# Kernel tuning notes

Hardware: AMD Instinct MI355X
Metric: run time of the kernel (lower is better)

## Reference

```python
import jax, jax.numpy as jnp
import numpy as np
import math

N, E, IN, C, H, ED, B = 50000, 800000, 64, 32, 4, 1, 64
HC = H * C
EPS = 1e-5


def setup_inputs() -> dict:
    key = jax.random.key(0)
    ks = jax.random.split(key, 16)
    def lin(k, fan_in, fan_out):
        s = 1.0 / math.sqrt(fan_in)
        return jax.random.normal(k, (fan_in, fan_out), jnp.float32) * s
    inp = {
        "x": jax.random.normal(ks[0], (N, IN), jnp.float32),
        "edge_index": jax.random.randint(ks[1], (2, E), 0, N, jnp.int64),
        "edge_attr": jax.random.normal(ks[2], (E, ED), jnp.float32),
        "batch_index": jnp.sort(jax.random.randint(ks[3], (N,), 0, B, jnp.int64)),
        # TransformerConv params
        "Wq": lin(ks[4], IN, HC), "bq": jnp.zeros((HC,), jnp.float32),
        "Wk": lin(ks[5], IN, HC), "bk": jnp.zeros((HC,), jnp.float32),
        "Wv": lin(ks[6], IN, HC), "bv": jnp.zeros((HC,), jnp.float32),
        "We": lin(ks[7], ED, HC), "be": jnp.zeros((HC,), jnp.float32),
        "Wskip": lin(ks[8], IN, HC), "bskip": jnp.zeros((HC,), jnp.float32),
        "Wbeta": lin(ks[9], 3 * HC, 1),
        # post linear: H*C -> C
        "Wlin": lin(ks[10], HC, C), "blin": jnp.zeros((C,), jnp.float32),
        # GraphNorm params
        "gn_weight": jnp.ones((C,), jnp.float32),
        "gn_bias": jnp.zeros((C,), jnp.float32),
        "gn_mean_scale": jnp.ones((C,), jnp.float32),
    }
    return inp


def reference(x, edge_index, edge_attr, batch_index, Wq, bq, Wk, bk, Wv, bv,
              We, be, Wskip, bskip, Wbeta, Wlin, blin,
              gn_weight, gn_bias, gn_mean_scale):
    src, dst = edge_index[0], edge_index[1]
    # dense projections [N, H, C]
    q = (x @ Wq + bq).reshape(N, H, C)
    k = (x @ Wk + bk).reshape(N, H, C)
    v = (x @ Wv + bv).reshape(N, H, C)
    e = (edge_attr @ We + be).reshape(E, H, C)
    # per-edge attention logits [E, H]
    k_e = k[src] + e
    alpha = jnp.einsum('ehc,ehc->eh', q[dst], k_e) / math.sqrt(C)
    # segment softmax over incoming edges of each dst node
    m = jax.ops.segment_max(alpha, dst, num_segments=N)  # [N, H]
    a = jnp.exp(alpha - m[dst])
    denom = jax.ops.segment_sum(a, dst, num_segments=N)  # [N, H]
    a = a / jnp.maximum(denom, 1e-16)[dst]
    # (dropout p=0.3 on attention is a no-op in eval mode)
    msg = (v[src] + e) * a[:, :, None]                    # [E, H, C]
    out = jax.ops.segment_sum(msg, dst, num_segments=N).reshape(N, HC)
    # beta-gated skip connection
    x_r = x @ Wskip + bskip                               # [N, HC]
    beta = jax.nn.sigmoid(jnp.concatenate([out, x_r, out - x_r], -1) @ Wbeta)
    out = beta * x_r + (1.0 - beta) * out
    # linear + relu
    h = jax.nn.relu(out @ Wlin + blin)                    # [N, C]
    # GraphNorm over per-graph segments
    ones = jnp.ones((N, 1), h.dtype)
    cnt = jax.ops.segment_sum(ones, batch_index, num_segments=B)  # [B, 1]
    cnt = jnp.maximum(cnt, 1.0)
    mean = jax.ops.segment_sum(h, batch_index, num_segments=B) / cnt
    centered = h - mean[batch_index] * gn_mean_scale
    var = jax.ops.segment_sum(centered * centered, batch_index, num_segments=B) / cnt
    std = jnp.sqrt(var + EPS)
    return gn_weight * centered / std[batch_index] + gn_bias
```

## Files before the change

### kernel.cpp

```cpp
#include <hip/hip_runtime.h>
#include <math.h>

static constexpr int kN  = 50000;
static constexpr int kE  = 800000;
static constexpr int kC  = 32;
static constexpr int kH  = 4;
static constexpr int kHC = 128;
static constexpr int kB  = 64;
static constexpr int kNB = (kN + 255) / 256;
static constexpr int kMB64 = (kN + 63) / 64;

typedef __attribute__((ext_vector_type(8))) short bf16x8;
typedef __attribute__((ext_vector_type(4))) float f32x4;

__device__ __forceinline__ unsigned short f2bf(float f) {
    unsigned u = __float_as_uint(f);
    unsigned r = (u + 0x7FFFu + ((u >> 16) & 1u)) >> 16;
    return (unsigned short)r;
}
__device__ __forceinline__ float blo(unsigned u) { return __uint_as_float(u << 16); }
__device__ __forceinline__ float bhi(unsigned u) { return __uint_as_float(u & 0xFFFF0000u); }

__global__ __launch_bounds__(256) void hist_packw_kernel(
    const int* __restrict__ ei, int* __restrict__ deg,
    const float* __restrict__ Wq, const float* __restrict__ Wk,
    const float* __restrict__ Wv, const float* __restrict__ Wskip,
    uint4* __restrict__ wtf)
{
    if (blockIdx.x < 16) {
        int tid = blockIdx.x * 256 + threadIdx.x;
        int f = tid >> 6, l = tid & 63;
        int m = f >> 4, c = (f >> 1) & 7, kk = f & 1;
        int col = c * 16 + (l & 15);
        int k0  = kk * 32 + (l >> 4) * 8;
        const float* Wm = (m == 0) ? Wq : (m == 1) ? Wk : (m == 2) ? Wv : Wskip;
        unsigned p[4];
#pragma unroll
        for (int j = 0; j < 4; ++j) {
            unsigned lo = f2bf(Wm[(k0 + 2 * j) * kHC + col]);
            unsigned hi = f2bf(Wm[(k0 + 2 * j + 1) * kHC + col]);
            p[j] = lo | (hi << 16);
        }
        wtf[f * 64 + l] = make_uint4(p[0], p[1], p[2], p[3]);
        return;
    }
    int i = (blockIdx.x - 16) * 256 + threadIdx.x;
    if (i < kE) atomicAdd(&deg[ei[kE + i]], 1);
}

__global__ __launch_bounds__(256) void proj_scanA_kernel(
    const float4* __restrict__ x4,
    const float* __restrict__ bq, const float* __restrict__ bk,
    const float* __restrict__ bv, const float* __restrict__ bskip,
    const uint4* __restrict__ wtf,
    unsigned short* __restrict__ qxb, unsigned short* __restrict__ kvb,
    const int* __restrict__ deg, int* __restrict__ bsum)
{
    __shared__ int sh4[4];
    if (blockIdx.x >= kMB64) {
        int bid = blockIdx.x - kMB64;
        int i = bid * 256 + threadIdx.x;
        int v = (i < kN) ? deg[i] : 0;
#pragma unroll
        for (int s = 1; s < 64; s <<= 1) v += __shfl_xor(v, s);
        if ((threadIdx.x & 63) == 0) sh4[threadIdx.x >> 6] = v;
        __syncthreads();
        if (threadIdx.x == 0) bsum[bid] = sh4[0] + sh4[1] + sh4[2] + sh4[3];
        return;
    }
    const int t = threadIdx.x;
    const int w = t >> 6;
    const int l = t & 63;
    const int l15 = l & 15, l16 = l >> 4;
    const int n0 = blockIdx.x * 64;

    bf16x8 bf[8][2];
#pragma unroll
    for (int c = 0; c < 8; ++c)
#pragma unroll
        for (int kk = 0; kk < 2; ++kk)
            bf[c][kk] = __builtin_bit_cast(bf16x8, wtf[(unsigned)((w * 16 + c * 2 + kk) * 64 + l)]);

    const float* Bm = (w == 0) ? bq : (w == 1) ? bk : (w == 2) ? bv : bskip;
    float bias[8];
#pragma unroll
    for (int c = 0; c < 8; ++c) bias[c] = Bm[c * 16 + l15];

    unsigned short* dst = (w == 0 || w == 3) ? qxb : kvb;
    const int add4 = (w >= 2) ? 4 : 0;

    for (int rt = 0; rt < 2; ++rt) {
        const int r0 = n0 + rt * 32 + l15;
        const int r1 = r0 + 16;
        f32x4 acc[2][8];
#pragma unroll
        for (int r = 0; r < 2; ++r)
#pragma unroll
            for (int c = 0; c < 8; ++c)
                acc[r][c] = (f32x4){bias[c], bias[c], bias[c], bias[c]};
#pragma unroll
        for (int kk = 0; kk < 2; ++kk) {
            float4 xa0 = make_float4(0.f,0.f,0.f,0.f), xb0 = xa0, xa1 = xa0, xb1 = xa0;
            if (r0 < kN) {
                xa0 = x4[(size_t)r0 * 16 + kk * 8 + l16 * 2];
                xb0 = x4[(size_t)r0 * 16 + kk * 8 + l16 * 2 + 1];
            }
            if (r1 < kN) {
                xa1 = x4[(size_t)r1 * 16 + kk * 8 + l16 * 2];
                xb1 = x4[(size_t)r1 * 16 + kk * 8 + l16 * 2 + 1];
            }
            uint4 u0 = make_uint4(
                f2bf(xa0.x) | ((unsigned)f2bf(xa0.y) << 16),
                f2bf(xa0.z) | ((unsigned)f2bf(xa0.w) << 16),
                f2bf(xb0.x) | ((unsigned)f2bf(xb0.y) << 16),
                f2bf(xb0.z) | ((unsigned)f2bf(xb0.w) << 16));
            uint4 u1 = make_uint4(
                f2bf(xa1.x) | ((unsigned)f2bf(xa1.y) << 16),
                f2bf(xa1.z) | ((unsigned)f2bf(xa1.w) << 16),
                f2bf(xb1.x) | ((unsigned)f2bf(xb1.y) << 16),
                f2bf(xb1.z) | ((unsigned)f2bf(xb1.w) << 16));
            bf16x8 a0 = __builtin_bit_cast(bf16x8, u0);
            bf16x8 a1 = __builtin_bit_cast(bf16x8, u1);
#pragma unroll
            for (int c = 0; c < 8; ++c) {
                acc[0][c] = __builtin_amdgcn_mfma_f32_16x16x32_bf16(a0, bf[c][kk], acc[0][c], 0, 0, 0);
                acc[1][c] = __builtin_amdgcn_mfma_f32_16x16x32_bf16(a1, bf[c][kk], acc[1][c], 0, 0, 0);
            }
        }
#pragma unroll
        for (int r = 0; r < 2; ++r) {
#pragma unroll
            for (int j = 0; j < 4; ++j) {
                int node = n0 + rt * 32 + r * 16 + l16 * 4 + j;
                bool valid = (node < kN) && ((l & 1) == 0);
                size_t base = (size_t)node * 128;
#pragma unroll
                for (int c = 0; c < 8; ++c) {
                    float v0 = acc[r][c][j];
                    float v1 = __shfl_xor(v0, 1);
                    if (valid) {
                        int jcol = c * 16 + l15;
                        int gpos = ((jcol >> 2) << 3) | (jcol & 3);
                        unsigned pk = f2bf(v0) | ((unsigned)f2bf(v1) << 16);
                        ((unsigned*)dst)[base + ((gpos + add4) >> 1)] = pk;
                    }
                }
            }
        }
    }
}

__global__ __launch_bounds__(256) void scanC2_kernel(
    const int* __restrict__ deg, const int* __restrict__ bsum,
    int* __restrict__ rowptr, int* __restrict__ cursor)
{
    __shared__ int bsh[256];
    __shared__ int sh[256];
    const int t = threadIdx.x, i = blockIdx.x * 256 + t;
    int bv = (t < kNB) ? bsum[t] : 0;
    bsh[t] = bv; __syncthreads();
    for (int off = 1; off < 256; off <<= 1) {
        int u = (t >= off) ? bsh[t - off] : 0;
        __syncthreads();
        bsh[t] += u;
        __syncthreads();
    }
    const int bofs = (blockIdx.x == 0) ? 0 : bsh[blockIdx.x - 1];
    if (blockIdx.x == 0 && t == 0) rowptr[kN] = bsh[kNB - 1];
    int v = (i < kN) ? deg[i] : 0;
    sh[t] = v; __syncthreads();
    for (int off = 1; off < 256; off <<= 1) {
        int u = (t >= off) ? sh[t - off] : 0;
        __syncthreads();
        sh[t] += u;
        __syncthreads();
    }
    if (i < kN) {
        int ex = sh[t] - v + bofs;
        rowptr[i] = ex;
        cursor[i] = ex;
    }
}

__global__ __launch_bounds__(256) void scatter_kernel(
    const int* __restrict__ ei, const float* __restrict__ ea,
    int* __restrict__ cursor, unsigned* __restrict__ csr)
{
    int i = blockIdx.x * 256 + threadIdx.x;
    if (i >= kE) return;
    int dst = ei[kE + i];
    int slot = atomicAdd(&cursor[dst], 1);
    csr[slot] = (unsigned)ei[i] | ((unsigned)f2bf(ea[i]) << 16);
}

__global__ __launch_bounds__(512) void node_attn_kernel(
    const int* __restrict__ rowptr, const unsigned* __restrict__ csr,
    const unsigned short* __restrict__ qxb, const unsigned short* __restrict__ kvb,
    const float* __restrict__ We, const float* __restrict__ be,
    const float* __restrict__ Wbeta, const float* __restrict__ Wlin,
    const float* __restrict__ blin, float* __restrict__ hbuf)
{
    __shared__ float wlS[kHC * kC];
    __shared__ float wbS[3 * kHC];
    __shared__ float oshS[8][kHC];
    const int t = threadIdx.x, wv = t >> 6, lane = t & 63;
    for (int i = t; i < kHC * kC; i += 512) wlS[i] = Wlin[i];
    for (int i = t; i < 3 * kHC; i += 512) wbS[i] = Wbeta[i];
    __syncthreads();

    const int node = blockIdx.x * 8 + wv;
    const int half = lane >> 5;
    const int sl   = lane & 31;
    const int ch   = sl * 4;
    const float4 we4 = *(const float4*)&We[ch];
    const float4 be4 = *(const float4*)&be[ch];
    const float4 wbA = *(const float4*)&wbS[ch];
    const float4 wbB = *(const float4*)&wbS[kHC + ch];
    const float4 wbC = *(const float4*)&wbS[2 * kHC + ch];
    const float blc = blin[sl];
    const float A2 = 0.17677669529663687f * 1.44269504088896341f;

    const uint4 qx = *((const uint4*)(qxb + (size_t)node * 256) + sl);
    const float q0 = blo(qx.x), q1 = bhi(qx.x), q2v = blo(qx.y), q3 = bhi(qx.y);
    const float xr0 = blo(qx.z), xr1 = bhi(qx.z), xr2 = blo(qx.w), xr3 = bhi(qx.w);
    float qw = q0 * we4.x + q1 * we4.y + q2v * we4.z + q3 * we4.w;
    float qe = q0 * be4.x + q1 * be4.y + q2v * be4.z + q3 * be4.w;
    qw += __shfl_xor(qw, 1); qe += __shfl_xor(qe, 1);
    qw += __shfl_xor(qw, 2); qe += __shfl_xor(qe, 2);
    qw += __shfl_xor(qw, 4); qe += __shfl_xor(qe, 4);
    const float qwA = qw * A2, qbA = qe * A2;

    float ss = 0.f, swa = 0.f;
    float ax0 = 0.f, ax1 = 0.f, ax2 = 0.f, ax3 = 0.f;
    const int beg = rowptr[node], end = rowptr[node + 1];
    int e = beg;
    for (; e + 3 < end; e += 4) {
        unsigned cA = csr[e + half];
        unsigned cB = csr[e + 2 + half];
        float aA = bhi(cA), aB = bhi(cB);
        const uint4 uA = *((const uint4*)(kvb + (size_t)(cA & 0xFFFFu) * 256) + sl);
        const uint4 uB = *((const uint4*)(kvb + (size_t)(cB & 0xFFFFu) * 256) + sl);
        float pA = fmaf(q3, bhi(uA.y), fmaf(q2v, blo(uA.y), fmaf(q1, bhi(uA.x), q0 * blo(uA.x))));
        float pB = fmaf(q3, bhi(uB.y), fmaf(q2v, blo(uB.y), fmaf(q1, bhi(uB.x), q0 * blo(uB.x))));
        pA += __shfl_xor(pA, 1); pB += __shfl_xor(pB, 1);
        pA += __shfl_xor(pA, 2); pB += __shfl_xor(pB, 2);
        pA += __shfl_xor(pA, 4); pB += __shfl_xor(pB, 4);
        float eA = __builtin_amdgcn_exp2f(fmaf(pA, A2, fmaf(aA, qwA, qbA)));
        float eB = __builtin_amdgcn_exp2f(fmaf(pB, A2, fmaf(aB, qwA, qbA)));
        ss  += eA + eB;
        swa = fmaf(eA, aA, fmaf(eB, aB, swa));
        ax0 = fmaf(eA, blo(uA.z), fmaf(eB, blo(uB.z), ax0));
        ax1 = fmaf(eA, bhi(uA.z), fmaf(eB, bhi(uB.z), ax1));
        ax2 = fmaf(eA, blo(uA.w), fmaf(eB, blo(uB.w), ax2));
        ax3 = fmaf(eA, bhi(uA.w), fmaf(eB, bhi(uB.w), ax3));
    }
    for (; e < end; e += 2) {
        int idx = e + half;
        bool valid = idx < end;
        unsigned cA = csr[valid ? idx : end - 1];
        float aA = bhi(cA);
        const uint4 uA = *((const uint4*)(kvb + (size_t)(cA & 0xFFFFu) * 256) + sl);
        float pA = fmaf(q3, bhi(uA.y), fmaf(q2v, blo(uA.y), fmaf(q1, bhi(uA.x), q0 * blo(uA.x))));
        pA += __shfl_xor(pA, 1);
        pA += __shfl_xor(pA, 2);
        pA += __shfl_xor(pA, 4);
        float eA = valid ? __builtin_amdgcn_exp2f(fmaf(pA, A2, fmaf(aA, qwA, qbA))) : 0.f;
        ss  += eA;
        swa = fmaf(eA, aA, swa);
        ax0 = fmaf(eA, blo(uA.z), ax0);
        ax1 = fmaf(eA, bhi(uA.z), ax1);
        ax2 = fmaf(eA, blo(uA.w), ax2);
        ax3 = fmaf(eA, bhi(uA.w), ax3);
    }
    ss  += __shfl_xor(ss , 32);
    swa += __shfl_xor(swa, 32);
    ax0 += __shfl_xor(ax0, 32);
    ax1 += __shfl_xor(ax1, 32);
    ax2 += __shfl_xor(ax2, 32);
    ax3 += __shfl_xor(ax3, 32);

    float rcp = 1.f / fmaxf(ss, 1e-16f);
    float v0 = fmaf(swa, we4.x, fmaf(ss, be4.x, ax0)) * rcp;
    float v1 = fmaf(swa, we4.y, fmaf(ss, be4.y, ax1)) * rcp;
    float v2 = fmaf(swa, we4.z, fmaf(ss, be4.z, ax2)) * rcp;
    float v3 = fmaf(swa, we4.w, fmaf(ss, be4.w, ax3)) * rcp;
    float part = wbA.x * v0 + wbA.y * v1 + wbA.z * v2 + wbA.w * v3
               + wbB.x * xr0 + wbB.y * xr1 + wbB.z * xr2 + wbB.w * xr3
               + wbC.x * (v0 - xr0) + wbC.y * (v1 - xr1)
               + wbC.z * (v2 - xr2) + wbC.w * (v3 - xr3);
    part += __shfl_xor(part, 1);
    part += __shfl_xor(part, 2);
    part += __shfl_xor(part, 4);
    part += __shfl_xor(part, 8);
    part += __shfl_xor(part, 16);
    float beta = 1.f / (1.f + __expf(-part));
    float o0 = beta * xr0 + (1.f - beta) * v0;
    float o1 = beta * xr1 + (1.f - beta) * v1;
    float o2 = beta * xr2 + (1.f - beta) * v2;
    float o3 = beta * xr3 + (1.f - beta) * v3;
    if (half == 0) *(float4*)&oshS[wv][ch] = make_float4(o0, o1, o2, o3);
    __builtin_amdgcn_wave_barrier();
    float hp = 0.f;
#pragma unroll
    for (int jj = 0; jj < 64; ++jj) {
        int j = half * 64 + jj;
        hp = fmaf(oshS[wv][j], wlS[j * kC + sl], hp);
    }
    hp += __shfl_xor(hp, 32);
    if (lane < 32) hbuf[(size_t)node * kC + sl] = fmaxf(hp + blc, 0.f);
}

__global__ __launch_bounds__(512) void gn_kernel(
    const float* __restrict__ hbuf, const int* __restrict__ batch,
    const float* __restrict__ gms,
    const float* __restrict__ gw, const float* __restrict__ gb,
    float* __restrict__ out)
{
    const int g = blockIdx.x;
    const int t = threadIdx.x;
    __shared__ int se[2];
    __shared__ float s1[16][kC], s2[16][kC];
    __shared__ float msS[kC], rsS[kC];
    if (t < 2) {
        int target = g + t;
        int lo = 0, hi = kN;
        while (lo < hi) { int mid = (lo + hi) >> 1; if (batch[mid] < target) lo = mid + 1; else hi = mid; }
        se[t] = lo;
    }
    __syncthreads();
    int start = se[0], end = se[1];
    float cnt = fmaxf((float)(end - start), 1.f);
    int c = t & 31, r = t >> 5;
    float a = 0.f, b = 0.f;
    for (int n = start + r; n < end; n += 16) {
        float v = hbuf[(size_t)n * kC + c];
        a += v; b = fmaf(v, v, b);
    }
    s1[r][c] = a; s2[r][c] = b;
    __syncthreads();
    if (t < kC) {
        float sa = 0.f, sb = 0.f;
#pragma unroll
        for (int i = 0; i < 16; ++i) { sa += s1[i][t]; sb += s2[i][t]; }
        float mean = sa / cnt;
        float ms   = mean * gms[t];
        float var  = sb / cnt - 2.f * ms * mean + ms * ms;
        msS[t] = ms;
        rsS[t] = rsqrtf(var + 1e-5f);
    }
    __syncthreads();
    float ms = msS[c], rs = rsS[c], w = gw[c], bb = gb[c];
    for (int n = start + r; n < end; n += 16) {
        float v = hbuf[(size_t)n * kC + c];
        out[(size_t)n * kC + c] = fmaf(w * (v - ms), rs, bb);
    }
}

extern "C" void kernel_launch(void* const* d_in, const int* in_sizes, int n_in,
                              void* d_out, int out_size, void* d_ws, size_t ws_size,
                              hipStream_t stream) {
    (void)in_sizes; (void)n_in; (void)out_size; (void)ws_size;
    const float* x     = (const float*)d_in[0];
    const int*   ei    = (const int*)d_in[1];
    const float* ea    = (const float*)d_in[2];
    const int*   batch = (const int*)d_in[3];
    const float* Wq    = (const float*)d_in[4];
    const float* bq    = (const float*)d_in[5];
    const float* Wk    = (const float*)d_in[6];
    const float* bk    = (const float*)d_in[7];
    const float* Wv    = (const float*)d_in[8];
    const float* bv    = (const float*)d_in[9];
    const float* We    = (const float*)d_in[10];
    const float* be    = (const float*)d_in[11];
    const float* Wskip = (const float*)d_in[12];
    const float* bskip = (const float*)d_in[13];
    const float* Wbeta = (const float*)d_in[14];
    const float* Wlin  = (const float*)d_in[15];
    const float* blin  = (const float*)d_in[16];
    const float* gw    = (const float*)d_in[17];
    const float* gb    = (const float*)d_in[18];
    const float* gms   = (const float*)d_in[19];
    float* out = (float*)d_out;

    char* ws = (char*)d_ws;
    unsigned* csr = (unsigned*)ws;        ws += (size_t)kE * 4;
    unsigned short* qxb = (unsigned short*)ws; ws += (size_t)kN * 256 * 2;
    unsigned short* kvb = (unsigned short*)ws; ws += (size_t)kN * 256 * 2;
    float* hbuf   = (float*)ws;           ws += (size_t)kN * kC * 4;
    int*   deg    = (int*)ws;             ws += (size_t)kN * 4;
    int*   cursor = (int*)ws;             ws += (size_t)kN * 4;
    int*   rowptr = (int*)ws;             ws += (size_t)(kN + 1) * 4;
    int*   bsum   = (int*)ws;             ws += (size_t)kNB * 4;
    uint4* wtf    = (uint4*)ws;           ws += (size_t)64 * 64 * 16;

    hipMemsetAsync(deg, 0, (size_t)kN * 4, stream);

    hist_packw_kernel<<<16 + (kE + 255) / 256, 256, 0, stream>>>(
        ei, deg, Wq, Wk, Wv, Wskip, wtf);
    proj_scanA_kernel<<<kMB64 + kNB, 256, 0, stream>>>(
        (const float4*)x, bq, bk, bv, bskip, wtf, qxb, kvb, deg, bsum);
    scanC2_kernel<<<kNB, 256, 0, stream>>>(deg, bsum, rowptr, cursor);
    scatter_kernel<<<(kE + 255) / 256, 256, 0, stream>>>(ei, ea, cursor, csr);
    node_attn_kernel<<<kN / 8, 512, 0, stream>>>(
        rowptr, csr, qxb, kvb, We, be, Wbeta, Wlin, blin, hbuf);
    gn_kernel<<<kB, 512, 0, stream>>>(hbuf, batch, gms, gw, gb, out);
}
```

Baseline: 222.2 us.

## Store keys as FP8 in a 384-byte KV row and fuse projection with scatter

```diff
diff --git a/kernel.cpp b/kernel.cpp
--- a/kernel.cpp
+++ b/kernel.cpp
@@ -9,9 +9,12 @@
 static constexpr int kB  = 64;
 static constexpr int kNB = (kN + 255) / 256;
 static constexpr int kMB64 = (kN + 63) / 64;
+static constexpr int kSB  = (kE + 255) / 256;
+static constexpr int kKVROW = 384;
 
 typedef __attribute__((ext_vector_type(8))) short bf16x8;
 typedef __attribute__((ext_vector_type(4))) float f32x4;
+typedef __attribute__((ext_vector_type(2))) float f32x2;
 
 __device__ __forceinline__ unsigned short f2bf(float f) {
     unsigned u = __float_as_uint(f);
@@ -48,24 +51,67 @@
     if (i < kE) atomicAdd(&deg[ei[kE + i]], 1);
 }
 
-__global__ __launch_bounds__(256) void proj_scanA_kernel(
+__global__ __launch_bounds__(256) void scanA_kernel(
+    const int* __restrict__ deg, int* __restrict__ bsum)
+{
+    __shared__ int sh4[4];
+    int i = blockIdx.x * 256 + threadIdx.x;
+    int v = (i < kN) ? deg[i] : 0;
+#pragma unroll
+    for (int s = 1; s < 64; s <<= 1) v += __shfl_xor(v, s);
+    if ((threadIdx.x & 63) == 0) sh4[threadIdx.x >> 6] = v;
+    __syncthreads();
+    if (threadIdx.x == 0) bsum[blockIdx.x] = sh4[0] + sh4[1] + sh4[2] + sh4[3];
+}
+
+__global__ __launch_bounds__(256) void scanC2_kernel(
+    const int* __restrict__ deg, const int* __restrict__ bsum,
+    int* __restrict__ rowptr, int* __restrict__ cursor)
+{
+    __shared__ int bsh[256];
+    __shared__ int sh[256];
+    const int t = threadIdx.x, i = blockIdx.x * 256 + t;
+    int bv = (t < kNB) ? bsum[t] : 0;
+    bsh[t] = bv; __syncthreads();
+    for (int off = 1; off < 256; off <<= 1) {
+        int u = (t >= off) ? bsh[t - off] : 0;
+        __syncthreads();
+        bsh[t] += u;
+        __syncthreads();
+    }
+    const int bofs = (blockIdx.x == 0) ? 0 : bsh[blockIdx.x - 1];
+    if (blockIdx.x == 0 && t == 0) rowptr[kN] = bsh[kNB - 1];
+    int v = (i < kN) ? deg[i] : 0;
+    sh[t] = v; __syncthreads();
+    for (int off = 1; off < 256; off <<= 1) {
+        int u = (t >= off) ? sh[t - off] : 0;
+        __syncthreads();
+        sh[t] += u;
+        __syncthreads();
+    }
+    if (i < kN) {
+        int ex = sh[t] - v + bofs;
+        rowptr[i] = ex;
+        cursor[i] = ex;
+    }
+}
+
+__global__ __launch_bounds__(256) void proj_scatter_kernel(
     const float4* __restrict__ x4,
     const float* __restrict__ bq, const float* __restrict__ bk,
     const float* __restrict__ bv, const float* __restrict__ bskip,
     const uint4* __restrict__ wtf,
-    unsigned short* __restrict__ qxb, unsigned short* __restrict__ kvb,
-    const int* __restrict__ deg, int* __restrict__ bsum)
-{
-    __shared__ int sh4[4];
+    unsigned short* __restrict__ qxb, unsigned char* __restrict__ kvb,
+    const int* __restrict__ ei, const float* __restrict__ ea,
+    int* __restrict__ cursor, unsigned* __restrict__ csr)
+{
     if (blockIdx.x >= kMB64) {
-        int bid = blockIdx.x - kMB64;
-        int i = bid * 256 + threadIdx.x;
-        int v = (i < kN) ? deg[i] : 0;
-#pragma unroll
-        for (int s = 1; s < 64; s <<= 1) v += __shfl_xor(v, s);
-        if ((threadIdx.x & 63) == 0) sh4[threadIdx.x >> 6] = v;
-        __syncthreads();
-        if (threadIdx.x == 0) bsum[bid] = sh4[0] + sh4[1] + sh4[2] + sh4[3];
+        int i = (blockIdx.x - kMB64) * 256 + threadIdx.x;
+        if (i < kE) {
+            int dst = ei[kE + i];
+            int slot = atomicAdd(&cursor[dst], 1);
+            csr[slot] = (unsigned)ei[i] | ((unsigned)f2bf(ea[i]) << 16);
+        }
         return;
     }
     const int t = threadIdx.x;
@@ -86,7 +132,6 @@
 #pragma unroll
     for (int c = 0; c < 8; ++c) bias[c] = Bm[c * 16 + l15];
 
-    unsigned short* dst = (w == 0 || w == 3) ? qxb : kvb;
     const int add4 = (w >= 2) ? 4 : 0;
 
     for (int rt = 0; rt < 2; ++rt) {
@@ -133,16 +178,24 @@
             for (int j = 0; j < 4; ++j) {
                 int node = n0 + rt * 32 + r * 16 + l16 * 4 + j;
                 bool valid = (node < kN) && ((l & 1) == 0);
-                size_t base = (size_t)node * 128;
 #pragma unroll
                 for (int c = 0; c < 8; ++c) {
                     float v0 = acc[r][c][j];
                     float v1 = __shfl_xor(v0, 1);
                     if (valid) {
                         int jcol = c * 16 + l15;
-                        int gpos = ((jcol >> 2) << 3) | (jcol & 3);
-                        unsigned pk = f2bf(v0) | ((unsigned)f2bf(v1) << 16);
-                        ((unsigned*)dst)[base + ((gpos + add4) >> 1)] = pk;
+                        if (w == 0 || w == 3) {
+                            int gpos = ((jcol >> 2) << 3) | (jcol & 3);
+                            unsigned pk = f2bf(v0) | ((unsigned)f2bf(v1) << 16);
+                            ((unsigned*)qxb)[(size_t)node * 128 + ((gpos + add4) >> 1)] = pk;
+                        } else if (w == 1) {
+                            unsigned short us = (unsigned short)
+                                __builtin_amdgcn_cvt_pk_fp8_f32(v0, v1, 0, false);
+                            *(unsigned short*)(kvb + (size_t)node * kKVROW + jcol) = us;
+                        } else {
+                            unsigned pk = f2bf(v0) | ((unsigned)f2bf(v1) << 16);
+                            *(unsigned*)(kvb + (size_t)node * kKVROW + 128 + 2 * jcol) = pk;
+                        }
                     }
                 }
             }
@@ -150,52 +203,9 @@
     }
 }
 
-__global__ __launch_bounds__(256) void scanC2_kernel(
-    const int* __restrict__ deg, const int* __restrict__ bsum,
-    int* __restrict__ rowptr, int* __restrict__ cursor)
-{
-    __shared__ int bsh[256];
-    __shared__ int sh[256];
-    const int t = threadIdx.x, i = blockIdx.x * 256 + t;
-    int bv = (t < kNB) ? bsum[t] : 0;
-    bsh[t] = bv; __syncthreads();
-    for (int off = 1; off < 256; off <<= 1) {
-        int u = (t >= off) ? bsh[t - off] : 0;
-        __syncthreads();
-        bsh[t] += u;
-        __syncthreads();
-    }
-    const int bofs = (blockIdx.x == 0) ? 0 : bsh[blockIdx.x - 1];
-    if (blockIdx.x == 0 && t == 0) rowptr[kN] = bsh[kNB - 1];
-    int v = (i < kN) ? deg[i] : 0;
-    sh[t] = v; __syncthreads();
-    for (int off = 1; off < 256; off <<= 1) {
-        int u = (t >= off) ? sh[t - off] : 0;
-        __syncthreads();
-        sh[t] += u;
-        __syncthreads();
-    }
-    if (i < kN) {
-        int ex = sh[t] - v + bofs;
-        rowptr[i] = ex;
-        cursor[i] = ex;
-    }
-}
-
-__global__ __launch_bounds__(256) void scatter_kernel(
-    const int* __restrict__ ei, const float* __restrict__ ea,
-    int* __restrict__ cursor, unsigned* __restrict__ csr)
-{
-    int i = blockIdx.x * 256 + threadIdx.x;
-    if (i >= kE) return;
-    int dst = ei[kE + i];
-    int slot = atomicAdd(&cursor[dst], 1);
-    csr[slot] = (unsigned)ei[i] | ((unsigned)f2bf(ea[i]) << 16);
-}
-
 __global__ __launch_bounds__(512) void node_attn_kernel(
     const int* __restrict__ rowptr, const unsigned* __restrict__ csr,
-    const unsigned short* __restrict__ qxb, const unsigned short* __restrict__ kvb,
+    const unsigned short* __restrict__ qxb, const unsigned char* __restrict__ kvb,
     const float* __restrict__ We, const float* __restrict__ be,
     const float* __restrict__ Wbeta, const float* __restrict__ Wlin,
     const float* __restrict__ blin, float* __restrict__ hbuf)
@@ -238,10 +248,18 @@
         unsigned cA = csr[e + half];
         unsigned cB = csr[e + 2 + half];
         float aA = bhi(cA), aB = bhi(cB);
-        const uint4 uA = *((const uint4*)(kvb + (size_t)(cA & 0xFFFFu) * 256) + sl);
-        const uint4 uB = *((const uint4*)(kvb + (size_t)(cB & 0xFFFFu) * 256) + sl);
-        float pA = fmaf(q3, bhi(uA.y), fmaf(q2v, blo(uA.y), fmaf(q1, bhi(uA.x), q0 * blo(uA.x))));
-        float pB = fmaf(q3, bhi(uB.y), fmaf(q2v, blo(uB.y), fmaf(q1, bhi(uB.x), q0 * blo(uB.x))));
+        const unsigned char* rA = kvb + (size_t)(cA & 0xFFFFu) * kKVROW;
+        const unsigned char* rB = kvb + (size_t)(cB & 0xFFFFu) * kKVROW;
+        unsigned kuA = *(const unsigned*)(rA + sl * 4);
+        unsigned kuB = *(const unsigned*)(rB + sl * 4);
+        uint2 vuA = *(const uint2*)(rA + 128 + sl * 8);
+        uint2 vuB = *(const uint2*)(rB + 128 + sl * 8);
+        f32x2 kA0 = __builtin_amdgcn_cvt_pk_f32_fp8(kuA, false);
+        f32x2 kA1 = __builtin_amdgcn_cvt_pk_f32_fp8(kuA, true);
+        f32x2 kB0 = __builtin_amdgcn_cvt_pk_f32_fp8(kuB, false);
+        f32x2 kB1 = __builtin_amdgcn_cvt_pk_f32_fp8(kuB, true);
+        float pA = fmaf(q3, kA1.y, fmaf(q2v, kA1.x, fmaf(q1, kA0.y, q0 * kA0.x)));
+        float pB = fmaf(q3, kB1.y, fmaf(q2v, kB1.x, fmaf(q1, kB0.y, q0 * kB0.x)));
         pA += __shfl_xor(pA, 1); pB += __shfl_xor(pB, 1);
         pA += __shfl_xor(pA, 2); pB += __shfl_xor(pB, 2);
         pA += __shfl_xor(pA, 4); pB += __shfl_xor(pB, 4);
@@ -249,28 +267,32 @@
         float eB = __builtin_amdgcn_exp2f(fmaf(pB, A2, fmaf(aB, qwA, qbA)));
         ss  += eA + eB;
         swa = fmaf(eA, aA, fmaf(eB, aB, swa));
-        ax0 = fmaf(eA, blo(uA.z), fmaf(eB, blo(uB.z), ax0));
-        ax1 = fmaf(eA, bhi(uA.z), fmaf(eB, bhi(uB.z), ax1));
-        ax2 = fmaf(eA, blo(uA.w), fmaf(eB, blo(uB.w), ax2));
-        ax3 = fmaf(eA, bhi(uA.w), fmaf(eB, bhi(uB.w), ax3));
+        ax0 = fmaf(eA, blo(vuA.x), fmaf(eB, blo(vuB.x), ax0));
+        ax1 = fmaf(eA, bhi(vuA.x), fmaf(eB, bhi(vuB.x), ax1));
+        ax2 = fmaf(eA, blo(vuA.y), fmaf(eB, blo(vuB.y), ax2));
+        ax3 = fmaf(eA, bhi(vuA.y), fmaf(eB, bhi(vuB.y), ax3));
     }
     for (; e < end; e += 2) {
         int idx = e + half;
         bool valid = idx < end;
         unsigned cA = csr[valid ? idx : end - 1];
         float aA = bhi(cA);
-        const uint4 uA = *((const uint4*)(kvb + (size_t)(cA & 0xFFFFu) * 256) + sl);
-        float pA = fmaf(q3, bhi(uA.y), fmaf(q2v, blo(uA.y), fmaf(q1, bhi(uA.x), q0 * blo(uA.x))));
+        const unsigned char* rA = kvb + (size_t)(cA & 0xFFFFu) * kKVROW;
+        unsigned kuA = *(const unsigned*)(rA + sl * 4);
+        uint2 vuA = *(const uint2*)(rA + 128 + sl * 8);
+        f32x2 kA0 = __builtin_amdgcn_cvt_pk_f32_fp8(kuA, false);
+        f32x2 kA1 = __builtin_amdgcn_cvt_pk_f32_fp8(kuA, true);
+        float pA = fmaf(q3, kA1.y, fmaf(q2v, kA1.x, fmaf(q1, kA0.y, q0 * kA0.x)));
         pA += __shfl_xor(pA, 1);
         pA += __shfl_xor(pA, 2);
         pA += __shfl_xor(pA, 4);
         float eA = valid ? __builtin_amdgcn_exp2f(fmaf(pA, A2, fmaf(aA, qwA, qbA))) : 0.f;
         ss  += eA;
         swa = fmaf(eA, aA, swa);
-        ax0 = fmaf(eA, blo(uA.z), ax0);
-        ax1 = fmaf(eA, bhi(uA.z), ax1);
-        ax2 = fmaf(eA, blo(uA.w), ax2);
-        ax3 = fmaf(eA, bhi(uA.w), ax3);
+        ax0 = fmaf(eA, blo(vuA.x), ax0);
+        ax1 = fmaf(eA, bhi(vuA.x), ax1);
+        ax2 = fmaf(eA, blo(vuA.y), ax2);
+        ax3 = fmaf(eA, bhi(vuA.y), ax3);
     }
     ss  += __shfl_xor(ss , 32);
     swa += __shfl_xor(swa, 32);
@@ -385,7 +407,7 @@
     char* ws = (char*)d_ws;
     unsigned* csr = (unsigned*)ws;        ws += (size_t)kE * 4;
     unsigned short* qxb = (unsigned short*)ws; ws += (size_t)kN * 256 * 2;
-    unsigned short* kvb = (unsigned short*)ws; ws += (size_t)kN * 256 * 2;
+    unsigned char* kvb = (unsigned char*)ws;   ws += (size_t)kN * kKVROW;
     float* hbuf   = (float*)ws;           ws += (size_t)kN * kC * 4;
     int*   deg    = (int*)ws;             ws += (size_t)kN * 4;
     int*   cursor = (int*)ws;             ws += (size_t)kN * 4;
@@ -395,12 +417,12 @@
 
     hipMemsetAsync(deg, 0, (size_t)kN * 4, stream);
 
-    hist_packw_kernel<<<16 + (kE + 255) / 256, 256, 0, stream>>>(
+    hist_packw_kernel<<<16 + kSB, 256, 0, stream>>>(
         ei, deg, Wq, Wk, Wv, Wskip, wtf);
-    proj_scanA_kernel<<<kMB64 + kNB, 256, 0, stream>>>(
-        (const float4*)x, bq, bk, bv, bskip, wtf, qxb, kvb, deg, bsum);
+    scanA_kernel<<<kNB, 256, 0, stream>>>(deg, bsum);
     scanC2_kernel<<<kNB, 256, 0, stream>>>(deg, bsum, rowptr, cursor);
-    scatter_kernel<<<(kE + 255) / 256, 256, 0, stream>>>(ei, ea, cursor, csr);
+    proj_scatter_kernel<<<kMB64 + kSB, 256, 0, stream>>>(
+        (const float4*)x, bq, bk, bv, bskip, wtf, qxb, kvb, ei, ea, cursor, csr);
     node_attn_kernel<<<kN / 8, 512, 0, stream>>>(
         rowptr, csr, qxb, kvb, We, be, Wbeta, Wlin, blin, hbuf);
     gn_kernel<<<kB, 512, 0, stream>>>(hbuf, batch, gms, gw, gb, out);
```

Measured after the change: 234.0 us. +5.3%, slower.
